# Performance work log

Measured on AMD Instinct MI355X. Metric: run time of the kernel, lower is better.

The kernel has to match this reference:

```python
import jax, jax.numpy as jnp
import numpy as np

D = 384
H = 6
DK = D // H
EPS = 1e-5


def _layernorm(x, g, b):
    mu = jnp.mean(x, axis=-1, keepdims=True)
    var = jnp.var(x, axis=-1, keepdims=True)
    return (x - mu) * jax.lax.rsqrt(var + EPS) * g + b


def setup_inputs() -> dict:
    key = jax.random.key(0)
    ks = jax.random.split(key, 12)
    B, N = 8, 2048
    s = lambda fan_in: 1.0 / np.sqrt(fan_in)
    return {
        "points": jax.random.normal(ks[0], (B, 3 + D, N), dtype=jnp.float32),
        "ln1_g": jnp.ones((D,), jnp.float32),
        "ln1_b": jnp.zeros((D,), jnp.float32),
        "w_qkv": jax.random.uniform(ks[1], (3 * D, D), jnp.float32, -s(D), s(D)),
        "w_o": jax.random.uniform(ks[2], (D, D), jnp.float32, -s(D), s(D)),
        "b_o": jnp.zeros((D,), jnp.float32),
        "ln2_g": jnp.ones((D,), jnp.float32),
        "ln2_b": jnp.zeros((D,), jnp.float32),
        "w1": jax.random.uniform(ks[3], (2 * D, D), jnp.float32, -s(D), s(D)),
        "b1": jnp.zeros((2 * D,), jnp.float32),
        "w2": jax.random.uniform(ks[4], (D, 2 * D), jnp.float32, -s(2 * D), s(2 * D)),
        "b2": jnp.zeros((D,), jnp.float32),
    }


def reference(points, ln1_g, ln1_b, w_qkv, w_o, b_o, ln2_g, ln2_b, w1, b1, w2, b2):
    coords = points[:, :3, :]                       # [B, 3, N]
    feats = jnp.transpose(points[:, 3:, :], (0, 2, 1))  # [B, N, D]
    B, N, _ = feats.shape

    # pre-norm + fused QKV projection (no bias)
    h = _layernorm(feats, ln1_g, ln1_b)
    qkv = jnp.einsum('bnd,ed->bne', h, w_qkv)       # [B, N, 3D]
    q, k, v = jnp.split(qkv, 3, axis=-1)

    split_heads = lambda t: jnp.transpose(t.reshape(B, N, H, DK), (0, 2, 1, 3))
    q, k, v = split_heads(q), split_heads(k), split_heads(v)  # [B, H, N, DK]

    scale = DK ** -0.5
    scores = jnp.einsum('bhid,bhjd->bhij', q, k) * scale      # [B, H, N, N]
    attn = jax.nn.softmax(scores, axis=-1)
    ctx = jnp.einsum('bhij,bhjd->bhid', attn, v)              # [B, H, N, DK]
    ctx = jnp.transpose(ctx, (0, 2, 1, 3)).reshape(B, N, D)
    attn_out = jnp.einsum('bnd,ed->bne', ctx, w_o) + b_o

    x = feats + attn_out
    # FFN with exact (erf) GELU, hidden = 2*D
    h2 = _layernorm(x, ln2_g, ln2_b)
    ff = jnp.einsum('bnd,ed->bne', h2, w1) + b1
    ff = jax.nn.gelu(ff, approximate=False)
    ff = jnp.einsum('bne,de->bnd', ff, w2) + b2
    x = x + ff

    return jnp.concatenate([coords, jnp.transpose(x, (0, 2, 1))], axis=1)
```

## Files before the change

kernel.cpp:

```cpp
#include <hip/hip_runtime.h>
#include <cstdint>


typedef __bf16 bf16;
typedef __bf16 bf16x8 __attribute__((ext_vector_type(8)));
typedef __bf16 bf16x4 __attribute__((ext_vector_type(4)));
typedef short s16x4 __attribute__((ext_vector_type(4)));
typedef float floatx4 __attribute__((ext_vector_type(4)));
typedef uint32_t __attribute__((address_space(1))) gu32;
typedef uint32_t __attribute__((address_space(3))) lu32;

#define NN 2048
#define DD 384
#define HH 6
#define DK 64
#define BB 8
#define MM (BB * NN)
#define D3 (3 * DD)
#define D2 (2 * DD)
#define CH (3 + DD)
#define LP 72

#define QSCALE 0.18033688011112042f

static __device__ __forceinline__ s16x4 as_s16x4(bf16x4 v) {
    union { bf16x4 b; s16x4 s; } u; u.b = v; return u.s;
}


__global__ void cast_all_kernel(const float* __restrict__ w_qkv, const float* __restrict__ w_o,
                                const float* __restrict__ w1, const float* __restrict__ w2,
                                bf16* __restrict__ o_qkv, bf16* __restrict__ o_o,
                                bf16* __restrict__ o_w1, bf16* __restrict__ o_w2) {
    int i = blockIdx.x * 256 + threadIdx.x;
    if (i < 442368) o_qkv[i] = (bf16)w_qkv[i];
    else if (i < 589824) o_o[i - 442368] = (bf16)w_o[i - 442368];
    else if (i < 884736) o_w1[i - 589824] = (bf16)w1[i - 589824];
    else o_w2[i - 884736] = (bf16)w2[i - 884736];
}

__global__ void coords_kernel(const float* __restrict__ pts, float* __restrict__ out) {
    int i = blockIdx.x * 256 + threadIdx.x;
    int b = i / (3 * NN), r = i % (3 * NN);
    out[(size_t)b * CH * NN + r] = pts[(size_t)b * CH * NN + r];
}

__global__ void transpose_kernel(const float* __restrict__ pts, float* __restrict__ feats) {
    __shared__ float T[32][33];
    int n0 = blockIdx.x * 32, d0 = blockIdx.y * 32, b = blockIdx.z;
    int tx = threadIdx.x, ty = threadIdx.y;
    const float* src = pts + (size_t)b * CH * NN;
#pragma unroll
    for (int i = 0; i < 4; ++i)
        T[ty + i * 8][tx] = src[(size_t)(3 + d0 + ty + i * 8) * NN + n0 + tx];
    __syncthreads();
    float* dst = feats + (size_t)b * NN * DD;
#pragma unroll
    for (int i = 0; i < 4; ++i)
        dst[(size_t)(n0 + ty + i * 8) * DD + d0 + tx] = T[tx][ty + i * 8];
}

__global__ __launch_bounds__(256) void ln_kernel(const float* __restrict__ x,
                                                 const float* __restrict__ g,
                                                 const float* __restrict__ bta,
                                                 bf16* __restrict__ out) {
    int wave = threadIdx.x >> 6, lane = threadIdx.x & 63;
    int row = blockIdx.x * 4 + wave;
    const float* xr = x + (size_t)row * DD;
    float v[6], s = 0.f, sq = 0.f;
#pragma unroll
    for (int i = 0; i < 6; ++i) { v[i] = xr[lane + i * 64]; s += v[i]; sq += v[i] * v[i]; }
#pragma unroll
    for (int o = 1; o < 64; o <<= 1) { s += __shfl_xor(s, o); sq += __shfl_xor(sq, o); }
    float mu = s * (1.f / DD);
    float var = sq * (1.f / DD) - mu * mu;
    float rs = rsqrtf(var + 1e-5f);
    bf16* orow = out + (size_t)row * DD;
#pragma unroll
    for (int i = 0; i < 6; ++i) {
        int d = lane + i * 64;
        orow[d] = (bf16)((v[i] - mu) * rs * g[d] + bta[d]);
    }
}

template <int NC, int K, int MODE>
__global__ __launch_bounds__(256, 2)
void gemm_bt(const bf16* __restrict__ A, const bf16* __restrict__ W,
             const float* __restrict__ bias, const float* __restrict__ res,
             bf16* __restrict__ obf, float* __restrict__ of32, bf16* __restrict__ vt) {
    __shared__ bf16 As[128 * 32];
    __shared__ bf16 Ws[128 * 32];
    const int t = threadIdx.x;
    const int wave = t >> 6, lane = t & 63;
    const int m0 = blockIdx.x * 128, n0 = blockIdx.y * 128;
    const int wm = (wave >> 1) * 64, wn = (wave & 1) * 64;
    const int lr = lane & 15, quad = lane >> 4;
    const int sr = t >> 2, sc = (t & 3) * 8;

    floatx4 acc[4][4];
#pragma unroll
    for (int mi = 0; mi < 4; ++mi)
#pragma unroll
        for (int ni = 0; ni < 4; ++ni) {
            floatx4 z = {0.f, 0.f, 0.f, 0.f};
            acc[mi][ni] = z;
        }

    for (int k0 = 0; k0 < K; k0 += 32) {
        __syncthreads();
#pragma unroll
        for (int i = 0; i < 2; ++i) {
            const int r = i * 64 + sr;
            __builtin_amdgcn_global_load_lds(
                (const gu32*)&A[(size_t)(m0 + r) * K + k0 + sc],
                (lu32*)&As[r * 32 + sc], 16, 0, 0);
            __builtin_amdgcn_global_load_lds(
                (const gu32*)&W[(size_t)(n0 + r) * K + k0 + sc],
                (lu32*)&Ws[r * 32 + sc], 16, 0, 0);
        }
        __syncthreads();
        bf16x8 af[4], bfr[4];
#pragma unroll
        for (int mi = 0; mi < 4; ++mi)
            af[mi] = *(const bf16x8*)&As[(wm + mi * 16 + lr) * 32 + quad * 8];
#pragma unroll
        for (int ni = 0; ni < 4; ++ni)
            bfr[ni] = *(const bf16x8*)&Ws[(wn + ni * 16 + lr) * 32 + quad * 8];
#pragma unroll
        for (int mi = 0; mi < 4; ++mi)
#pragma unroll
            for (int ni = 0; ni < 4; ++ni)
                acc[mi][ni] = __builtin_amdgcn_mfma_f32_16x16x32_bf16(af[mi], bfr[ni], acc[mi][ni], 0, 0, 0);
    }

#pragma unroll
    for (int mi = 0; mi < 4; ++mi) {
#pragma unroll
        for (int ni = 0; ni < 4; ++ni) {
            const int r0 = m0 + wm + mi * 16 + quad * 4;
            const int c = n0 + wn + ni * 16 + lr;
            floatx4 v = acc[mi][ni];
            if constexpr (MODE == 0) {
                const int cb = n0 + wn + ni * 16;
                if (cb >= 2 * DD) {
                    const int hh = (c - 2 * DD) >> 6, dk = (c - 2 * DD) & 63;
                    const int b = r0 >> 11, n = r0 & (NN - 1);
                    bf16x4 pk;
#pragma unroll
                    for (int r = 0; r < 4; ++r) pk[r] = (bf16)v[r];
                    *(bf16x4*)&vt[((size_t)(b * HH + hh) * DK + dk) * NN + n] = pk;
                } else {
                    const float sc_q = (cb < DD) ? QSCALE : 1.0f;
#pragma unroll
                    for (int r = 0; r < 4; ++r) obf[(size_t)(r0 + r) * NC + c] = (bf16)(v[r] * sc_q);
                }
            } else if constexpr (MODE == 1) {
#pragma unroll
                for (int r = 0; r < 4; ++r)
                    of32[(size_t)(r0 + r) * NC + c] = v[r] + bias[c] + res[(size_t)(r0 + r) * NC + c];
            } else if constexpr (MODE == 2) {
#pragma unroll
                for (int r = 0; r < 4; ++r) {
                    float u = v[r] + bias[c];
                    obf[(size_t)(r0 + r) * NC + c] = (bf16)(0.5f * u * (1.f + erff(u * 0.70710678118f)));
                }
            } else {
                const int b = r0 >> 11, n = r0 & (NN - 1);
                float o4[4];
#pragma unroll
                for (int r = 0; r < 4; ++r)
                    o4[r] = v[r] + bias[c] + res[(size_t)(r0 + r) * DD + c];
                float4 val = make_float4(o4[0], o4[1], o4[2], o4[3]);
                *(float4*)&of32[((size_t)b * CH + 3 + c) * NN + n] = val;
            }
        }
    }
}

__global__ __launch_bounds__(256, 4)
void attn_kernel(const bf16* __restrict__ qkv, const bf16* __restrict__ vt,
                 bf16* __restrict__ ctx) {
    __shared__ bf16 Ks[64 * LP];
    __shared__ bf16 Vs[64 * LP];
    const int t = threadIdx.x, wave = t >> 6, lane = t & 63;
    const int lr = lane & 15, quad = lane >> 4;
    const int bh = blockIdx.y, b = bh / HH, h = bh % HH;
    const int q0 = blockIdx.x * 128;
    const bf16* qbase = qkv + (size_t)b * NN * D3 + h * DK;
    const bf16* kbase = qbase + DD;
    const bf16* vbase = vt + (size_t)bh * DK * NN;

    bf16x8 aq[2][2];
#pragma unroll
    for (int mi = 0; mi < 2; ++mi)
#pragma unroll
        for (int ks = 0; ks < 2; ++ks)
            aq[mi][ks] = *(const bf16x8*)&qbase[(size_t)(q0 + wave * 32 + mi * 16 + lr) * D3 +
                                                ks * 32 + quad * 8];

    bf16x4 ones4;
#pragma unroll
    for (int i = 0; i < 4; ++i) ones4[i] = (bf16)1.0f;
    const s16x4 ones_s = as_s16x4(ones4);

    floatx4 o[2][4], ol[2];
#pragma unroll
    for (int mi = 0; mi < 2; ++mi) {
        floatx4 z = {0.f, 0.f, 0.f, 0.f};
        ol[mi] = z;
#pragma unroll
        for (int nd = 0; nd < 4; ++nd) o[mi][nd] = z;
    }

    for (int j0 = 0; j0 < NN; j0 += 64) {
        __syncthreads();
        {
            const int rr = t >> 3, cc = (t & 7) * 8;
#pragma unroll
            for (int i = 0; i < 2; ++i) {
                const int j = i * 32 + rr;
                *(bf16x8*)&Ks[j * LP + cc] =
                    *(const bf16x8*)&kbase[(size_t)(j0 + j) * D3 + cc];
                *(bf16x8*)&Vs[j * LP + cc] =
                    *(const bf16x8*)&vbase[(size_t)j * NN + j0 + cc];
            }
        }
        __syncthreads();

        floatx4 s[2][4];
#pragma unroll
        for (int mi = 0; mi < 2; ++mi)
#pragma unroll
            for (int nj = 0; nj < 4; ++nj) {
                floatx4 z = {0.f, 0.f, 0.f, 0.f};
                s[mi][nj] = z;
            }
#pragma unroll
        for (int ks = 0; ks < 2; ++ks)
#pragma unroll
            for (int nj = 0; nj < 4; ++nj) {
                bf16x8 bk = *(const bf16x8*)&Ks[(nj * 16 + lr) * LP + ks * 32 + quad * 8];
#pragma unroll
                for (int mi = 0; mi < 2; ++mi)
                    s[mi][nj] = __builtin_amdgcn_mfma_f32_16x16x32_bf16(bk, aq[mi][ks], s[mi][nj], 0, 0, 0);
            }

#pragma unroll
        for (int nj = 0; nj < 4; ++nj) {
            s16x4 ap[2];
#pragma unroll
            for (int mi = 0; mi < 2; ++mi) {
                bf16x4 pk;
#pragma unroll
                for (int r = 0; r < 4; ++r) pk[r] = (bf16)exp2f(s[mi][nj][r]);
                ap[mi] = as_s16x4(pk);
            }
#pragma unroll
            for (int nd = 0; nd < 4; ++nd) {
                s16x4 bv = as_s16x4(*(const bf16x4*)&Vs[(nd * 16 + lr) * LP + nj * 16 + quad * 4]);
#pragma unroll
                for (int mi = 0; mi < 2; ++mi)
                    o[mi][nd] = __builtin_amdgcn_mfma_f32_16x16x16bf16_1k(ap[mi], bv, o[mi][nd], 0, 0, 0);
            }
#pragma unroll
            for (int mi = 0; mi < 2; ++mi)
                ol[mi] = __builtin_amdgcn_mfma_f32_16x16x16bf16_1k(ap[mi], ones_s, ol[mi], 0, 0, 0);
        }
    }

#pragma unroll
    for (int mi = 0; mi < 2; ++mi)
#pragma unroll
        for (int r = 0; r < 4; ++r) {
            const int n = q0 + wave * 32 + mi * 16 + quad * 4 + r;
            const float inv = 1.0f / ol[mi][r];
#pragma unroll
            for (int nd = 0; nd < 4; ++nd) {
                const int d = h * DK + nd * 16 + lr;
                ctx[(size_t)(b * NN + n) * DD + d] = (bf16)(o[mi][nd][r] * inv);
            }
        }
}


extern "C" void kernel_launch(void* const* d_in, const int* in_sizes, int n_in,
                              void* d_out, int out_size, void* d_ws, size_t ws_size,
                              hipStream_t stream) {
    const float* points = (const float*)d_in[0];
    const float* ln1_g = (const float*)d_in[1];
    const float* ln1_b = (const float*)d_in[2];
    const float* w_qkv = (const float*)d_in[3];
    const float* w_o   = (const float*)d_in[4];
    const float* b_o   = (const float*)d_in[5];
    const float* ln2_g = (const float*)d_in[6];
    const float* ln2_b = (const float*)d_in[7];
    const float* w1    = (const float*)d_in[8];
    const float* b1    = (const float*)d_in[9];
    const float* w2    = (const float*)d_in[10];
    const float* b2    = (const float*)d_in[11];
    float* out = (float*)d_out;

    char* ws = (char*)d_ws;
    size_t off = 0;
    auto alloc = [&](size_t bytes) -> void* {
        void* p = ws + off;
        off += (bytes + 255) & ~(size_t)255;
        return p;
    };
    float* feats = (float*)alloc((size_t)MM * DD * 4);
    float* xbuf  = (float*)alloc((size_t)MM * DD * 4);
    bf16* h1     = (bf16*)alloc((size_t)MM * DD * 2);
    bf16* h2     = (bf16*)alloc((size_t)MM * DD * 2);
    bf16* qkvb   = (bf16*)alloc((size_t)MM * D3 * 2);
    bf16* vtb    = (bf16*)alloc((size_t)BB * HH * DK * NN * 2);
    bf16* ctx    = (bf16*)alloc((size_t)MM * DD * 2);
    bf16* ffh    = (bf16*)alloc((size_t)MM * D2 * 2);
    bf16* wqkv_bf = (bf16*)alloc((size_t)D3 * DD * 2);
    bf16* wo_bf   = (bf16*)alloc((size_t)DD * DD * 2);
    bf16* w1_bf   = (bf16*)alloc((size_t)D2 * DD * 2);
    bf16* w2_bf   = (bf16*)alloc((size_t)DD * D2 * 2);

    cast_all_kernel<<<1179648 / 256, 256, 0, stream>>>(w_qkv, w_o, w1, w2,
                                                       wqkv_bf, wo_bf, w1_bf, w2_bf);
    coords_kernel<<<(BB * 3 * NN) / 256, 256, 0, stream>>>(points, out);
    transpose_kernel<<<dim3(NN / 32, DD / 32, BB), dim3(32, 8), 0, stream>>>(points, feats);
    ln_kernel<<<MM / 4, 256, 0, stream>>>(feats, ln1_g, ln1_b, h1);
    gemm_bt<D3, DD, 0><<<dim3(MM / 128, D3 / 128), 256, 0, stream>>>(
        h1, wqkv_bf, nullptr, nullptr, qkvb, nullptr, vtb);
    attn_kernel<<<dim3(NN / 128, BB * HH), 256, 0, stream>>>(qkvb, vtb, ctx);
    gemm_bt<DD, DD, 1><<<dim3(MM / 128, DD / 128), 256, 0, stream>>>(
        ctx, wo_bf, b_o, feats, nullptr, xbuf, nullptr);
    ln_kernel<<<MM / 4, 256, 0, stream>>>(xbuf, ln2_g, ln2_b, h2);
    gemm_bt<D2, DD, 2><<<dim3(MM / 128, D2 / 128), 256, 0, stream>>>(
        h2, w1_bf, b1, nullptr, ffh, nullptr, nullptr);
    gemm_bt<DD, D2, 3><<<dim3(MM / 128, DD / 128), 256, 0, stream>>>(
        ffh, w2_bf, b2, xbuf, nullptr, out, nullptr);
}
```

Before: 299.7 us.

## Load attention K/V fragments directly from global and narrow GEMM N-tiles

The attention kernel drops its shared-memory K/V staging and both block barriers. Each wave now loads its K and V^T MFMA fragments straight from global memory into registers, relying on L1/L2 to serve the reuse across the four waves. The GEMM kernel gains a TN template parameter, and the two N=384 projections use 64-wide N tiles so more blocks are launched and the GPU is better occupied. The cost is redundant global/cache traffic in attention, higher register pressure (launch bound lowered to 3 blocks per SM), and less reuse per block in the narrower GEMMs.

```diff
diff --git a/kernel.cpp b/kernel.cpp
--- a/kernel.cpp
+++ b/kernel.cpp
@@ -19,7 +19,6 @@
 #define D3 (3 * DD)
 #define D2 (2 * DD)
 #define CH (3 + DD)
-#define LP 72
 
 #define QSCALE 0.18033688011112042f
 
@@ -83,23 +82,25 @@
     }
 }
 
-template <int NC, int K, int MODE>
+template <int NC, int K, int MODE, int TN>
 __global__ __launch_bounds__(256, 2)
 void gemm_bt(const bf16* __restrict__ A, const bf16* __restrict__ W,
              const float* __restrict__ bias, const float* __restrict__ res,
              bf16* __restrict__ obf, float* __restrict__ of32, bf16* __restrict__ vt) {
+    constexpr int MI = (TN == 128) ? 4 : 2;
     __shared__ bf16 As[128 * 32];
-    __shared__ bf16 Ws[128 * 32];
+    __shared__ bf16 Ws[TN * 32];
     const int t = threadIdx.x;
     const int wave = t >> 6, lane = t & 63;
-    const int m0 = blockIdx.x * 128, n0 = blockIdx.y * 128;
-    const int wm = (wave >> 1) * 64, wn = (wave & 1) * 64;
+    const int m0 = blockIdx.x * 128, n0 = blockIdx.y * TN;
+    const int wm = (TN == 128) ? (wave >> 1) * 64 : wave * 32;
+    const int wn = (TN == 128) ? (wave & 1) * 64 : 0;
     const int lr = lane & 15, quad = lane >> 4;
     const int sr = t >> 2, sc = (t & 3) * 8;
 
-    floatx4 acc[4][4];
-#pragma unroll
-    for (int mi = 0; mi < 4; ++mi)
+    floatx4 acc[MI][4];
+#pragma unroll
+    for (int mi = 0; mi < MI; ++mi)
 #pragma unroll
         for (int ni = 0; ni < 4; ++ni) {
             floatx4 z = {0.f, 0.f, 0.f, 0.f};
@@ -114,27 +115,31 @@
             __builtin_amdgcn_global_load_lds(
                 (const gu32*)&A[(size_t)(m0 + r) * K + k0 + sc],
                 (lu32*)&As[r * 32 + sc], 16, 0, 0);
+        }
+#pragma unroll
+        for (int i = 0; i < TN / 64; ++i) {
+            const int r = i * 64 + sr;
             __builtin_amdgcn_global_load_lds(
                 (const gu32*)&W[(size_t)(n0 + r) * K + k0 + sc],
                 (lu32*)&Ws[r * 32 + sc], 16, 0, 0);
         }
         __syncthreads();
-        bf16x8 af[4], bfr[4];
-#pragma unroll
-        for (int mi = 0; mi < 4; ++mi)
+        bf16x8 af[MI], bfr[4];
+#pragma unroll
+        for (int mi = 0; mi < MI; ++mi)
             af[mi] = *(const bf16x8*)&As[(wm + mi * 16 + lr) * 32 + quad * 8];
 #pragma unroll
         for (int ni = 0; ni < 4; ++ni)
             bfr[ni] = *(const bf16x8*)&Ws[(wn + ni * 16 + lr) * 32 + quad * 8];
 #pragma unroll
-        for (int mi = 0; mi < 4; ++mi)
+        for (int mi = 0; mi < MI; ++mi)
 #pragma unroll
             for (int ni = 0; ni < 4; ++ni)
                 acc[mi][ni] = __builtin_amdgcn_mfma_f32_16x16x32_bf16(af[mi], bfr[ni], acc[mi][ni], 0, 0, 0);
     }
 
 #pragma unroll
-    for (int mi = 0; mi < 4; ++mi) {
+    for (int mi = 0; mi < MI; ++mi) {
 #pragma unroll
         for (int ni = 0; ni < 4; ++ni) {
             const int r0 = m0 + wm + mi * 16 + quad * 4;
@@ -177,15 +182,13 @@
     }
 }
 
-__global__ __launch_bounds__(256, 4)
+__global__ __launch_bounds__(256, 3)
 void attn_kernel(const bf16* __restrict__ qkv, const bf16* __restrict__ vt,
                  bf16* __restrict__ ctx) {
-    __shared__ bf16 Ks[64 * LP];
-    __shared__ bf16 Vs[64 * LP];
     const int t = threadIdx.x, wave = t >> 6, lane = t & 63;
     const int lr = lane & 15, quad = lane >> 4;
     const int bh = blockIdx.y, b = bh / HH, h = bh % HH;
-    const int q0 = blockIdx.x * 128;
+    const int q0 = blockIdx.x * 128 + wave * 32;
     const bf16* qbase = qkv + (size_t)b * NN * D3 + h * DK;
     const bf16* kbase = qbase + DD;
     const bf16* vbase = vt + (size_t)bh * DK * NN;
@@ -195,7 +198,7 @@
     for (int mi = 0; mi < 2; ++mi)
 #pragma unroll
         for (int ks = 0; ks < 2; ++ks)
-            aq[mi][ks] = *(const bf16x8*)&qbase[(size_t)(q0 + wave * 32 + mi * 16 + lr) * D3 +
+            aq[mi][ks] = *(const bf16x8*)&qbase[(size_t)(q0 + mi * 16 + lr) * D3 +
                                                 ks * 32 + quad * 8];
 
     bf16x4 ones4;
@@ -213,19 +216,20 @@
     }
 
     for (int j0 = 0; j0 < NN; j0 += 64) {
-        __syncthreads();
-        {
-            const int rr = t >> 3, cc = (t & 7) * 8;
-#pragma unroll
-            for (int i = 0; i < 2; ++i) {
-                const int j = i * 32 + rr;
-                *(bf16x8*)&Ks[j * LP + cc] =
-                    *(const bf16x8*)&kbase[(size_t)(j0 + j) * D3 + cc];
-                *(bf16x8*)&Vs[j * LP + cc] =
-                    *(const bf16x8*)&vbase[(size_t)j * NN + j0 + cc];
-            }
-        }
-        __syncthreads();
+        bf16x8 bk[2][4];
+#pragma unroll
+        for (int ks = 0; ks < 2; ++ks)
+#pragma unroll
+            for (int nj = 0; nj < 4; ++nj)
+                bk[ks][nj] = *(const bf16x8*)&kbase[(size_t)(j0 + nj * 16 + lr) * D3 +
+                                                    ks * 32 + quad * 8];
+        s16x4 bv[4][4];
+#pragma unroll
+        for (int nd = 0; nd < 4; ++nd)
+#pragma unroll
+            for (int nj = 0; nj < 4; ++nj)
+                bv[nd][nj] = as_s16x4(*(const bf16x4*)&vbase[(size_t)(nd * 16 + lr) * NN +
+                                                             j0 + nj * 16 + quad * 4]);
 
         floatx4 s[2][4];
 #pragma unroll
@@ -238,12 +242,11 @@
 #pragma unroll
         for (int ks = 0; ks < 2; ++ks)
 #pragma unroll
-            for (int nj = 0; nj < 4; ++nj) {
-                bf16x8 bk = *(const bf16x8*)&Ks[(nj * 16 + lr) * LP + ks * 32 + quad * 8];
+            for (int nj = 0; nj < 4; ++nj)
 #pragma unroll
                 for (int mi = 0; mi < 2; ++mi)
-                    s[mi][nj] = __builtin_amdgcn_mfma_f32_16x16x32_bf16(bk, aq[mi][ks], s[mi][nj], 0, 0, 0);
-            }
+                    s[mi][nj] = __builtin_amdgcn_mfma_f32_16x16x32_bf16(bk[ks][nj], aq[mi][ks],
+                                                                        s[mi][nj], 0, 0, 0);
 
 #pragma unroll
         for (int nj = 0; nj < 4; ++nj) {
@@ -256,12 +259,11 @@
                 ap[mi] = as_s16x4(pk);
             }
 #pragma unroll
-            for (int nd = 0; nd < 4; ++nd) {
-                s16x4 bv = as_s16x4(*(const bf16x4*)&Vs[(nd * 16 + lr) * LP + nj * 16 + quad * 4]);
+            for (int nd = 0; nd < 4; ++nd)
 #pragma unroll
                 for (int mi = 0; mi < 2; ++mi)
-                    o[mi][nd] = __builtin_amdgcn_mfma_f32_16x16x16bf16_1k(ap[mi], bv, o[mi][nd], 0, 0, 0);
-            }
+                    o[mi][nd] = __builtin_amdgcn_mfma_f32_16x16x16bf16_1k(ap[mi], bv[nd][nj],
+                                                                          o[mi][nd], 0, 0, 0);
 #pragma unroll
             for (int mi = 0; mi < 2; ++mi)
                 ol[mi] = __builtin_amdgcn_mfma_f32_16x16x16bf16_1k(ap[mi], ones_s, ol[mi], 0, 0, 0);
@@ -272,7 +274,7 @@
     for (int mi = 0; mi < 2; ++mi)
 #pragma unroll
         for (int r = 0; r < 4; ++r) {
-            const int n = q0 + wave * 32 + mi * 16 + quad * 4 + r;
+            const int n = q0 + mi * 16 + quad * 4 + r;
             const float inv = 1.0f / ol[mi][r];
 #pragma unroll
             for (int nd = 0; nd < 4; ++nd) {
@@ -325,14 +327,14 @@
     coords_kernel<<<(BB * 3 * NN) / 256, 256, 0, stream>>>(points, out);
     transpose_kernel<<<dim3(NN / 32, DD / 32, BB), dim3(32, 8), 0, stream>>>(points, feats);
     ln_kernel<<<MM / 4, 256, 0, stream>>>(feats, ln1_g, ln1_b, h1);
-    gemm_bt<D3, DD, 0><<<dim3(MM / 128, D3 / 128), 256, 0, stream>>>(
+    gemm_bt<D3, DD, 0, 128><<<dim3(MM / 128, D3 / 128), 256, 0, stream>>>(
         h1, wqkv_bf, nullptr, nullptr, qkvb, nullptr, vtb);
     attn_kernel<<<dim3(NN / 128, BB * HH), 256, 0, stream>>>(qkvb, vtb, ctx);
-    gemm_bt<DD, DD, 1><<<dim3(MM / 128, DD / 128), 256, 0, stream>>>(
+    gemm_bt<DD, DD, 1, 64><<<dim3(MM / 128, DD / 64), 256, 0, stream>>>(
         ctx, wo_bf, b_o, feats, nullptr, xbuf, nullptr);
     ln_kernel<<<MM / 4, 256, 0, stream>>>(xbuf, ln2_g, ln2_b, h2);
-    gemm_bt<D2, DD, 2><<<dim3(MM / 128, D2 / 128), 256, 0, stream>>>(
+    gemm_bt<D2, DD, 2, 128><<<dim3(MM / 128, D2 / 128), 256, 0, stream>>>(
         h2, w1_bf, b1, nullptr, ffh, nullptr, nullptr);
-    gemm_bt<DD, D2, 3><<<dim3(MM / 128, DD / 128), 256, 0, stream>>>(
+    gemm_bt<DD, D2, 3, 64><<<dim3(MM / 128, DD / 64), 256, 0, stream>>>(
         ffh, w2_bf, b2, xbuf, nullptr, out, nullptr);
 }
```

New measurement: 458.3 us. 52.9% more time.
